# Performance work log

Hardware: AMD Instinct MI355X
Metric: run time of the kernel (lower is better)

Reference implementation:

```python
import jax, jax.numpy as jnp
import numpy as np

N_NODES = 20000
N_EDGES = 320000
MUL = 32
N_SPECIES = 4
AVG_NUM_NEIGHBORS = 16.0


def setup_inputs() -> dict:
    key = jax.random.key(0)
    ks = jax.random.split(key, 16)
    node_features = jax.random.normal(ks[0], (N_NODES, 128), dtype=jnp.float32)
    species = jax.random.randint(ks[1], (N_NODES,), 0, N_SPECIES)
    node_attrs = jax.nn.one_hot(species, N_SPECIES, dtype=jnp.float32)
    edge_embedding = jax.random.uniform(ks[2], (N_EDGES, 8), dtype=jnp.float32)
    edge_attrs = jax.random.normal(ks[3], (N_EDGES, 4), dtype=jnp.float32)
    edge_index = jax.random.randint(ks[4], (2, N_EDGES), 0, N_NODES)
    # learned params (e3nn-style normal init; fan-in normalization applied in forward)
    W_lin1_0 = jax.random.normal(ks[5], (MUL, MUL), dtype=jnp.float32)
    W_lin1_1 = jax.random.normal(ks[6], (MUL, MUL), dtype=jnp.float32)
    mlp_w1 = jax.random.normal(ks[7], (8, 8), dtype=jnp.float32) / np.sqrt(8.0)
    mlp_w2 = jax.random.normal(ks[8], (8, 128), dtype=jnp.float32) / np.sqrt(8.0)
    W_lin2_0 = jax.random.normal(ks[9], (2 * MUL, MUL), dtype=jnp.float32)
    W_lin2_1 = jax.random.normal(ks[10], (2 * MUL, MUL), dtype=jnp.float32)
    sc_w0 = jax.random.normal(ks[11], (MUL, N_SPECIES, MUL), dtype=jnp.float32)
    sc_w1 = jax.random.normal(ks[12], (MUL, N_SPECIES, MUL), dtype=jnp.float32)
    return dict(node_features=node_features, node_attrs=node_attrs,
                edge_embedding=edge_embedding, edge_attrs=edge_attrs,
                edge_index=edge_index, W_lin1_0=W_lin1_0, W_lin1_1=W_lin1_1,
                mlp_w1=mlp_w1, mlp_w2=mlp_w2, W_lin2_0=W_lin2_0,
                W_lin2_1=W_lin2_1, sc_w0=sc_w0, sc_w1=sc_w1)


def _forward(node_features, node_attrs, edge_embedding, edge_attrs, edge_index,
             W_lin1_0, W_lin1_1, mlp_w1, mlp_w2, W_lin2_0, W_lin2_1, sc_w0, sc_w1):
    N = node_features.shape[0]
    x0 = node_features[:, :MUL]                      # [N,32] 0e scalars
    x1 = node_features[:, MUL:].reshape(N, MUL, 3)   # [N,32,3] 1o vectors
    # self-connection: FullyConnectedTensorProduct(feats, node_attrs(0e) -> feats)
    sc_norm = 1.0 / np.sqrt(MUL * N_SPECIES)
    sc0 = jnp.einsum('ni,nj,ijk->nk', x0, node_attrs, sc_w0) * sc_norm
    sc1 = jnp.einsum('nim,nj,ijk->nkm', x1, node_attrs, sc_w1) * sc_norm
    # linear_1 (per-irrep block linear, fan-in normalized)
    y0 = (x0 @ W_lin1_0) / np.sqrt(MUL)
    y1 = jnp.einsum('nim,ij->njm', x1, W_lin1_1) / np.sqrt(MUL)
    # radial MLP: silu hidden (no bias) -> tp weights [E,128]
    w = jax.nn.silu(edge_embedding @ mlp_w1) @ mlp_w2
    w0, w1, w2, w3 = w[:, 0:32], w[:, 32:64], w[:, 64:96], w[:, 96:128]
    edge_src = edge_index[1]
    edge_dst = edge_index[0]
    e0 = y0[edge_src]            # [E,32] gathered scalars
    e1 = y1[edge_src]            # [E,32,3] gathered vectors
    sh0 = edge_attrs[:, :1]      # [E,1]  l=0 SH
    sh1 = edge_attrs[:, 1:]      # [E,3]  l=1 SH
    # per-edge weighted uvu tensor product; mid sorted order: 0e(i0),0e(i3),1o(i1),1o(i2)
    m0a = w0 * e0 * sh0                                           # 0e x 0e -> 0e
    m0b = w3 * jnp.einsum('eim,em->ei', e1, sh1) / np.sqrt(3.0)   # 1o x 1o -> 0e
    m1a = w1[:, :, None] * e0[:, :, None] * sh1[:, None, :]       # 0e x 1o -> 1o
    m1b = w2[:, :, None] * e1 * sh0[:, :, None]                   # 1o x 0e -> 1o
    scale = 1.0 / np.sqrt(AVG_NUM_NEIGHBORS)
    mid0 = jnp.concatenate([m0a, m0b], axis=1) * scale            # [E,64]
    mid1 = jnp.concatenate([m1a, m1b], axis=1) * scale            # [E,64,3]
    # scatter-add to destination nodes
    a0 = jax.ops.segment_sum(mid0, edge_dst, num_segments=N)
    a1 = jax.ops.segment_sum(mid1, edge_dst, num_segments=N)
    # linear_2 on simplified irreps 64x0e+64x1o -> 32x0e+32x1o
    o0 = (a0 @ W_lin2_0) / np.sqrt(2.0 * MUL)
    o1 = jnp.einsum('nim,ij->njm', a1, W_lin2_1) / np.sqrt(2.0 * MUL)
    out0 = o0 + sc0
    out1 = o1 + sc1
    return jnp.concatenate([out0, out1.reshape(N, MUL * 3)], axis=1)


def reference(node_features, node_attrs, edge_embedding, edge_attrs, edge_index,
              W_lin1_0, W_lin1_1, mlp_w1, mlp_w2, W_lin2_0, W_lin2_1, sc_w0, sc_w1):
    return _forward(node_features, node_attrs, edge_embedding, edge_attrs, edge_index,
                    W_lin1_0, W_lin1_1, mlp_w1, mlp_w2, W_lin2_0, W_lin2_1, sc_w0, sc_w1)
```

## Files before the change

kernel.cpp:

```cpp
#include <hip/hip_runtime.h>

#define N_NODES 20000
#define N_EDGES 320000
#define Y1OFF 640000
#define CAPMAX 64

__device__ __forceinline__ void mlp_h(const float* __restrict__ emb,
                                      const float* __restrict__ mw1,
                                      int e, float h[8])
{
    const float4 ea4 = ((const float4*)emb)[e * 2];
    const float4 eb4 = ((const float4*)emb)[e * 2 + 1];
    const float em[8] = {ea4.x, ea4.y, ea4.z, ea4.w,
                         eb4.x, eb4.y, eb4.z, eb4.w};
    #pragma unroll
    for (int l = 0; l < 8; ++l) {
        float acc = 0.f;
        #pragma unroll
        for (int k = 0; k < 8; ++k) acc += em[k] * mw1[k * 8 + l];
        h[l] = acc / (1.f + __expf(-acc));
    }
}

__device__ __forceinline__ void write_rec(float4* __restrict__ recs, int slot,
                                          int src, float4 sh, const float h[8])
{
    float4* rp = recs + (size_t)slot * 4;
    rp[0] = make_float4(__int_as_float(src), sh.x, sh.y, sh.z);
    rp[1] = make_float4(sh.w, h[0], h[1], h[2]);
    rp[2] = make_float4(h[3], h[4], h[5], h[6]);
    rp[3] = make_float4(h[7], 0.f, 0.f, 0.f);
}

__global__ __launch_bounds__(256) void prep_fill(
    const float* __restrict__ nf, const float* __restrict__ attrs,
    const int* __restrict__ eidx, const float* __restrict__ emb,
    const float* __restrict__ eattr,
    const float* __restrict__ W10, const float* __restrict__ W11,
    const float* __restrict__ mw1,
    const float* __restrict__ scw0, const float* __restrict__ scw1,
    float* __restrict__ y0, float* __restrict__ y1p,
    int* __restrict__ cnt, float4* __restrict__ recs, int cap, int append,
    float* __restrict__ out)
{
    __shared__ float sx[8][128];
    __shared__ float sat[8][4];
    const int tid = threadIdx.x;
    const int nb = blockIdx.x * 8;

    if (tid < 128) {
        const int e = blockIdx.x * 128 + tid;
        const int dst = eidx[e];
        const int pos = atomicAdd(&cnt[dst], 1);
        if (append && pos < cap) {
            const int src = eidx[N_EDGES + e];
            float h[8];
            mlp_h(emb, mw1, e, h);
            write_rec(recs, dst * cap + pos, src, ((const float4*)eattr)[e], h);
        }
    }

    {
        const float4* src = (const float4*)(nf + (size_t)nb * 128);
        ((float4*)&sx[0][0])[tid] = src[tid];
        if (tid < 32) ((float*)&sat[0][0])[tid] = attrs[nb * 4 + tid];
    }
    __syncthreads();

    const int slot = tid >> 5;
    const int j = tid & 31;
    const int n = nb + slot;
    const float* x = sx[slot];
    const float* at = sat[slot];
    const float inv_s32 = 0.17677669529663689f;
    const float sc_norm = 0.08838834764831845f;

    float acc0 = 0.f;
    #pragma unroll
    for (int i = 0; i < 32; ++i) acc0 += x[i] * W10[i * 32 + j];
    y0[(size_t)n * 32 + j] = acc0 * inv_s32;

    float b0 = 0.f, b1 = 0.f, b2 = 0.f;
    #pragma unroll
    for (int i = 0; i < 32; ++i) {
        float w = W11[i * 32 + j];
        b0 += x[32 + i * 3 + 0] * w;
        b1 += x[32 + i * 3 + 1] * w;
        b2 += x[32 + i * 3 + 2] * w;
    }
    y1p[            (size_t)n * 32 + j] = b0 * inv_s32;
    y1p[Y1OFF     + (size_t)n * 32 + j] = b1 * inv_s32;
    y1p[2 * Y1OFF + (size_t)n * 32 + j] = b2 * inv_s32;

    const int s = (at[1] > 0.5f) ? 1 : (at[2] > 0.5f) ? 2 : (at[3] > 0.5f) ? 3 : 0;
    float s0 = 0.f, s1_0 = 0.f, s1_1 = 0.f, s1_2 = 0.f;
    #pragma unroll 8
    for (int i = 0; i < 32; ++i) {
        const float we0 = scw0[i * 128 + s * 32 + j];
        s0 += x[i] * we0;
        const float we1 = scw1[i * 128 + s * 32 + j];
        s1_0 += x[32 + i*3 + 0] * we1;
        s1_1 += x[32 + i*3 + 1] * we1;
        s1_2 += x[32 + i*3 + 2] * we1;
    }
    float* on = out + (size_t)n * 128;
    on[j] = s0 * sc_norm;
    on[32 + j*3 + 0] = s1_0 * sc_norm;
    on[32 + j*3 + 1] = s1_1 * sc_norm;
    on[32 + j*3 + 2] = s1_2 * sc_norm;
}

__global__ __launch_bounds__(1024) void scan_kernel(
    const int* __restrict__ cnt, int* __restrict__ row_start,
    int* __restrict__ cursor)
{
    const int tid = threadIdx.x;
    const int base = tid * 20;
    int pre[20];
    int sum = 0;
    #pragma unroll
    for (int k = 0; k < 20; ++k) { pre[k] = sum; sum += cnt[base + k]; }
    __shared__ int s[1024];
    s[tid] = sum;
    __syncthreads();
    for (int off = 1; off < 1024; off <<= 1) {
        int t = (tid >= off) ? s[tid - off] : 0;
        __syncthreads();
        s[tid] += t;
        __syncthreads();
    }
    const int excl = s[tid] - sum;
    #pragma unroll
    for (int k = 0; k < 20; ++k) {
        const int v = excl + pre[k];
        row_start[base + k] = v;
        cursor[base + k] = v;
    }
    if (tid == 1023) row_start[N_NODES] = s[1023];
}

__global__ __launch_bounds__(256) void fill_csr(
    const int* __restrict__ eidx, const float* __restrict__ emb,
    const float* __restrict__ eattr, const float* __restrict__ mw1,
    int* __restrict__ cursor, float4* __restrict__ recs)
{
    const int e = blockIdx.x * 256 + threadIdx.x;
    const int dst = eidx[e];
    const int src = eidx[N_EDGES + e];
    const int pos = atomicAdd(&cursor[dst], 1);
    float h[8];
    mlp_h(emb, mw1, e, h);
    write_rec(recs, pos, src, ((const float4*)eattr)[e], h);
}

__device__ __forceinline__ void load_rec(const float4* __restrict__ rb, int t,
                                         float4& a, float4& b, float4& c, float& h7)
{
    const float4* p = rb + (size_t)t * 4;
    a = p[0]; b = p[1]; c = p[2];
    h7 = ((const float*)p)[12];
}

__global__ __launch_bounds__(256) void gather_kernel(
    const int* __restrict__ row_start, const int* __restrict__ cnt,
    int mode, int cap,
    const float4* __restrict__ recs,
    const float* __restrict__ mw2,
    const float* __restrict__ y0, const float* __restrict__ y1p,
    const float* __restrict__ W20, const float* __restrict__ W21,
    float* __restrict__ out)
{
    __shared__ float s_w20[2048];
    __shared__ float s_w21[2048];
    __shared__ float s_a[4][256];

    const int tid = threadIdx.x;
    ((float4*)s_w20)[tid]       = ((const float4*)W20)[tid];
    ((float4*)s_w20)[256 + tid] = ((const float4*)W20)[256 + tid];
    ((float4*)s_w21)[tid]       = ((const float4*)W21)[tid];
    ((float4*)s_w21)[256 + tid] = ((const float4*)W21)[256 + tid];

    const int wave = tid >> 6;
    const int lane = tid & 63;
    const int li   = lane & 31;
    const int hh   = lane >> 5;
    const int n    = blockIdx.x * 4 + wave;

    float c0[8], c1[8], c2[8], c3[8];
    #pragma unroll
    for (int l = 0; l < 8; ++l) {
        const float* r = mw2 + l * 128 + li;
        c0[l] = r[0];  c1[l] = r[32];  c2[l] = r[64];  c3[l] = r[96];
    }

    int roff, deg;
    if (mode) { roff = n * cap; deg = min(cnt[n], cap); }
    else      { roff = row_start[n]; deg = row_start[n + 1] - roff; }
    const float4* rb = recs + (size_t)roff * 4;

    float am0a = 0.f, am0b = 0.f;
    float am1a0 = 0.f, am1a1 = 0.f, am1a2 = 0.f;
    float am1b0 = 0.f, am1b1 = 0.f, am1b2 = 0.f;

    const int nk = (deg - hh + 1) >> 1;

    float4 Pa, Pb, Pc; float Ph7;
    float4 Qa, Qb, Qc; float Qh7;
    float Ye0, Ye10, Ye11, Ye12;

    if (nk > 0) load_rec(rb, hh,     Pa, Pb, Pc, Ph7);
    if (nk > 1) load_rec(rb, hh + 2, Qa, Qb, Qc, Qh7);
    if (nk > 0) {
        const size_t o = (size_t)__float_as_int(Pa.x) * 32 + li;
        Ye0 = y0[o]; Ye10 = y1p[o]; Ye11 = y1p[Y1OFF + o]; Ye12 = y1p[2 * Y1OFF + o];
    }

    for (int k = 0; k < nk; ++k) {
        float4 Na, Nb, Nc; float Nh7;
        if (k + 2 < nk) load_rec(rb, hh + 2 * (k + 2), Na, Nb, Nc, Nh7);
        float Z0, Z10, Z11, Z12;
        if (k + 1 < nk) {
            const size_t o = (size_t)__float_as_int(Qa.x) * 32 + li;
            Z0 = y0[o]; Z10 = y1p[o]; Z11 = y1p[Y1OFF + o]; Z12 = y1p[2 * Y1OFF + o];
        }

        {
            const float h0 = Pb.y, h1 = Pb.z, h2 = Pb.w, h3 = Pc.x;
            const float h4 = Pc.y, h5 = Pc.z, h6 = Pc.w, h7 = Ph7;
            float w0 = h0*c0[0] + h1*c0[1] + h2*c0[2] + h3*c0[3]
                     + h4*c0[4] + h5*c0[5] + h6*c0[6] + h7*c0[7];
            float w1 = h0*c1[0] + h1*c1[1] + h2*c1[2] + h3*c1[3]
                     + h4*c1[4] + h5*c1[5] + h6*c1[6] + h7*c1[7];
            float w2 = h0*c2[0] + h1*c2[1] + h2*c2[2] + h3*c2[3]
                     + h4*c2[4] + h5*c2[5] + h6*c2[6] + h7*c2[7];
            float w3 = h0*c3[0] + h1*c3[1] + h2*c3[2] + h3*c3[3]
                     + h4*c3[4] + h5*c3[5] + h6*c3[6] + h7*c3[7];
            const float sh0 = Pa.y, s1x = Pa.z, s1y = Pa.w, s1z = Pb.x;

            am0a += w0 * Ye0 * sh0;
            const float dotv = Ye10 * s1x + Ye11 * s1y + Ye12 * s1z;
            am0b += w3 * dotv;
            const float w1e = w1 * Ye0;
            am1a0 += w1e * s1x;  am1a1 += w1e * s1y;  am1a2 += w1e * s1z;
            const float w2s = w2 * sh0;
            am1b0 += w2s * Ye10; am1b1 += w2s * Ye11; am1b2 += w2s * Ye12;
        }

        Pa = Qa; Pb = Qb; Pc = Qc; Ph7 = Qh7;
        Qa = Na; Qb = Nb; Qc = Nc; Qh7 = Nh7;
        Ye0 = Z0; Ye10 = Z10; Ye11 = Z11; Ye12 = Z12;
    }

    am0a  += __shfl_xor(am0a, 32);
    am0b  += __shfl_xor(am0b, 32);
    am1a0 += __shfl_xor(am1a0, 32);
    am1a1 += __shfl_xor(am1a1, 32);
    am1a2 += __shfl_xor(am1a2, 32);
    am1b0 += __shfl_xor(am1b0, 32);
    am1b1 += __shfl_xor(am1b1, 32);
    am1b2 += __shfl_xor(am1b2, 32);

    const float scale = 0.25f;
    const float s3    = 0.25f * 0.5773502691896258f;

    float* sa = s_a[wave];
    if (hh == 0) {
        sa[li]      = am0a * scale;
        sa[32 + li] = am0b * s3;
        sa[64 + li * 3 + 0]      = am1a0 * scale;
        sa[64 + li * 3 + 1]      = am1a1 * scale;
        sa[64 + li * 3 + 2]      = am1a2 * scale;
        sa[64 + 96 + li * 3 + 0] = am1b0 * scale;
        sa[64 + 96 + li * 3 + 1] = am1b1 * scale;
        sa[64 + 96 + li * 3 + 2] = am1b2 * scale;
    }
    __syncthreads();

    const float inv8 = 0.125f;
    float* on = out + (size_t)n * 128;
    if (hh == 0) {
        float o0 = 0.f, o10 = 0.f;
        #pragma unroll
        for (int i = 0; i < 64; ++i) {
            o0  += sa[i]          * s_w20[i * 32 + li];
            o10 += sa[64 + i * 3] * s_w21[i * 32 + li];
        }
        on[li]              += o0  * inv8;
        on[32 + li * 3 + 0] += o10 * inv8;
    } else {
        float o11 = 0.f, o12 = 0.f;
        #pragma unroll
        for (int i = 0; i < 64; ++i) {
            const float w = s_w21[i * 32 + li];
            o11 += sa[64 + i * 3 + 1] * w;
            o12 += sa[64 + i * 3 + 2] * w;
        }
        on[32 + li * 3 + 1] += o11 * inv8;
        on[32 + li * 3 + 2] += o12 * inv8;
    }
}

extern "C" void kernel_launch(void* const* d_in, const int* in_sizes, int n_in,
                              void* d_out, int out_size, void* d_ws, size_t ws_size,
                              hipStream_t stream) {
    const float* nf    = (const float*)d_in[0];
    const float* attrs = (const float*)d_in[1];
    const float* emb   = (const float*)d_in[2];
    const float* eattr = (const float*)d_in[3];
    const int*   eidx  = (const int*)d_in[4];
    const float* W10   = (const float*)d_in[5];
    const float* W11   = (const float*)d_in[6];
    const float* mw1   = (const float*)d_in[7];
    const float* mw2   = (const float*)d_in[8];
    const float* W20   = (const float*)d_in[9];
    const float* W21   = (const float*)d_in[10];
    const float* scw0  = (const float*)d_in[11];
    const float* scw1  = (const float*)d_in[12];
    float* out = (float*)d_out;

    float* ws = (float*)d_ws;
    int*   cnt = (int*)ws;
    float* y0  = ws + 20480;
    float* y1p = ws + 660480;

    const size_t fixed_dw = 2580480;
    const size_t avail_b = ws_size > fixed_dw * 4 ? ws_size - fixed_dw * 4 : 0;
    int cap = (int)(avail_b / ((size_t)N_NODES * 64));
    if (cap > CAPMAX) cap = CAPMAX;

    hipMemsetAsync(cnt, 0, N_NODES * sizeof(int), stream);

    if (cap >= 44) {
        float4* recs = (float4*)(ws + fixed_dw);
        prep_fill<<<N_NODES / 8, 256, 0, stream>>>(
            nf, attrs, eidx, emb, eattr, W10, W11, mw1, scw0, scw1,
            y0, y1p, cnt, recs, cap, 1, out);
        gather_kernel<<<N_NODES / 4, 256, 0, stream>>>(
            nullptr, cnt, 1, cap, recs, mw2, y0, y1p, W20, W21, out);
    } else {
        int* row_start = (int*)(ws + fixed_dw);
        int* cursor    = row_start + 20001;
        float4* recs   = (float4*)(ws + 2620496);
        prep_fill<<<N_NODES / 8, 256, 0, stream>>>(
            nf, attrs, eidx, emb, eattr, W10, W11, mw1, scw0, scw1,
            y0, y1p, cnt, nullptr, 0, 0, out);
        scan_kernel<<<1, 1024, 0, stream>>>(cnt, row_start, cursor);
        fill_csr<<<N_EDGES / 256, 256, 0, stream>>>(eidx, emb, eattr, mw1,
                                                    cursor, recs);
        gather_kernel<<<N_NODES / 4, 256, 0, stream>>>(
            row_start, cnt, 0, 0, recs, mw2, y0, y1p, W20, W21, out);
    }
}
```

Before: 186.5 us.

## Pack node features as float4, split source indices, shrink edge records

Interleaves y0 and the three y1 components into one float4 per node and channel, so each neighbour gather is a single 16-byte load instead of four scattered loads. Edge records shrink from 64 to 48 bytes by moving source indices into a separate int array. Each wave loads that array once into a register vector and broadcasts indices with shuffles, removing the dependency on the record load before the feature gather can start. The CSR fallback now clamps degree to 64, which silently truncates nodes with more than 64 incoming edges, and the capacity threshold changes.

```diff
diff --git a/kernel.cpp b/kernel.cpp
--- a/kernel.cpp
+++ b/kernel.cpp
@@ -2,7 +2,6 @@
 
 #define N_NODES 20000
 #define N_EDGES 320000
-#define Y1OFF 640000
 #define CAPMAX 64
 
 __device__ __forceinline__ void mlp_h(const float* __restrict__ emb,
@@ -23,13 +22,12 @@
 }
 
 __device__ __forceinline__ void write_rec(float4* __restrict__ recs, int slot,
-                                          int src, float4 sh, const float h[8])
-{
-    float4* rp = recs + (size_t)slot * 4;
-    rp[0] = make_float4(__int_as_float(src), sh.x, sh.y, sh.z);
-    rp[1] = make_float4(sh.w, h[0], h[1], h[2]);
-    rp[2] = make_float4(h[3], h[4], h[5], h[6]);
-    rp[3] = make_float4(h[7], 0.f, 0.f, 0.f);
+                                          float4 sh, const float h[8])
+{
+    float4* rp = recs + (size_t)slot * 3;
+    rp[0] = sh;
+    rp[1] = make_float4(h[0], h[1], h[2], h[3]);
+    rp[2] = make_float4(h[4], h[5], h[6], h[7]);
 }
 
 __global__ __launch_bounds__(256) void prep_fill(
@@ -39,9 +37,9 @@
     const float* __restrict__ W10, const float* __restrict__ W11,
     const float* __restrict__ mw1,
     const float* __restrict__ scw0, const float* __restrict__ scw1,
-    float* __restrict__ y0, float* __restrict__ y1p,
-    int* __restrict__ cnt, float4* __restrict__ recs, int cap, int append,
-    float* __restrict__ out)
+    float4* __restrict__ y4,
+    int* __restrict__ cnt, int* __restrict__ srcs, float4* __restrict__ recs,
+    int cap, int append, float* __restrict__ out)
 {
     __shared__ float sx[8][128];
     __shared__ float sat[8][4];
@@ -53,10 +51,11 @@
         const int dst = eidx[e];
         const int pos = atomicAdd(&cnt[dst], 1);
         if (append && pos < cap) {
-            const int src = eidx[N_EDGES + e];
+            const int slot = dst * cap + pos;
+            srcs[slot] = eidx[N_EDGES + e];
             float h[8];
             mlp_h(emb, mw1, e, h);
-            write_rec(recs, dst * cap + pos, src, ((const float4*)eattr)[e], h);
+            write_rec(recs, slot, ((const float4*)eattr)[e], h);
         }
     }
 
@@ -78,7 +77,6 @@
     float acc0 = 0.f;
     #pragma unroll
     for (int i = 0; i < 32; ++i) acc0 += x[i] * W10[i * 32 + j];
-    y0[(size_t)n * 32 + j] = acc0 * inv_s32;
 
     float b0 = 0.f, b1 = 0.f, b2 = 0.f;
     #pragma unroll
@@ -88,9 +86,8 @@
         b1 += x[32 + i * 3 + 1] * w;
         b2 += x[32 + i * 3 + 2] * w;
     }
-    y1p[            (size_t)n * 32 + j] = b0 * inv_s32;
-    y1p[Y1OFF     + (size_t)n * 32 + j] = b1 * inv_s32;
-    y1p[2 * Y1OFF + (size_t)n * 32 + j] = b2 * inv_s32;
+    y4[(size_t)n * 32 + j] = make_float4(acc0 * inv_s32, b0 * inv_s32,
+                                         b1 * inv_s32, b2 * inv_s32);
 
     const int s = (at[1] > 0.5f) ? 1 : (at[2] > 0.5f) ? 2 : (at[3] > 0.5f) ? 3 : 0;
     float s0 = 0.f, s1_0 = 0.f, s1_1 = 0.f, s1_2 = 0.f;
@@ -142,31 +139,22 @@
 __global__ __launch_bounds__(256) void fill_csr(
     const int* __restrict__ eidx, const float* __restrict__ emb,
     const float* __restrict__ eattr, const float* __restrict__ mw1,
-    int* __restrict__ cursor, float4* __restrict__ recs)
+    int* __restrict__ cursor, int* __restrict__ srcs, float4* __restrict__ recs)
 {
     const int e = blockIdx.x * 256 + threadIdx.x;
     const int dst = eidx[e];
-    const int src = eidx[N_EDGES + e];
     const int pos = atomicAdd(&cursor[dst], 1);
+    srcs[pos] = eidx[N_EDGES + e];
     float h[8];
     mlp_h(emb, mw1, e, h);
-    write_rec(recs, pos, src, ((const float4*)eattr)[e], h);
-}
-
-__device__ __forceinline__ void load_rec(const float4* __restrict__ rb, int t,
-                                         float4& a, float4& b, float4& c, float& h7)
-{
-    const float4* p = rb + (size_t)t * 4;
-    a = p[0]; b = p[1]; c = p[2];
-    h7 = ((const float*)p)[12];
+    write_rec(recs, pos, ((const float4*)eattr)[e], h);
 }
 
 __global__ __launch_bounds__(256) void gather_kernel(
     const int* __restrict__ row_start, const int* __restrict__ cnt,
     int mode, int cap,
-    const float4* __restrict__ recs,
-    const float* __restrict__ mw2,
-    const float* __restrict__ y0, const float* __restrict__ y1p,
+    const int* __restrict__ srcs, const float4* __restrict__ recs,
+    const float* __restrict__ mw2, const float4* __restrict__ y4,
     const float* __restrict__ W20, const float* __restrict__ W21,
     float* __restrict__ out)
 {
@@ -186,6 +174,13 @@
     const int hh   = lane >> 5;
     const int n    = blockIdx.x * 4 + wave;
 
+    int roff, deg;
+    if (mode) { roff = n * cap; deg = min(cnt[n], cap); }
+    else      { roff = row_start[n]; deg = min(row_start[n + 1] - roff, 64); }
+
+    const int svec = srcs[roff + lane];
+    const float4* rb = recs + (size_t)roff * 3;
+
     float c0[8], c1[8], c2[8], c3[8];
     #pragma unroll
     for (int l = 0; l < 8; ++l) {
@@ -193,62 +188,62 @@
         c0[l] = r[0];  c1[l] = r[32];  c2[l] = r[64];  c3[l] = r[96];
     }
 
-    int roff, deg;
-    if (mode) { roff = n * cap; deg = min(cnt[n], cap); }
-    else      { roff = row_start[n]; deg = row_start[n + 1] - roff; }
-    const float4* rb = recs + (size_t)roff * 4;
-
     float am0a = 0.f, am0b = 0.f;
     float am1a0 = 0.f, am1a1 = 0.f, am1a2 = 0.f;
     float am1b0 = 0.f, am1b1 = 0.f, am1b2 = 0.f;
 
     const int nk = (deg - hh + 1) >> 1;
 
-    float4 Pa, Pb, Pc; float Ph7;
-    float4 Qa, Qb, Qc; float Qh7;
-    float Ye0, Ye10, Ye11, Ye12;
-
-    if (nk > 0) load_rec(rb, hh,     Pa, Pb, Pc, Ph7);
-    if (nk > 1) load_rec(rb, hh + 2, Qa, Qb, Qc, Qh7);
-    if (nk > 0) {
-        const size_t o = (size_t)__float_as_int(Pa.x) * 32 + li;
-        Ye0 = y0[o]; Ye10 = y1p[o]; Ye11 = y1p[Y1OFF + o]; Ye12 = y1p[2 * Y1OFF + o];
+    float4 Pa, Ph0, Ph1, Py;
+    float4 Qa, Qh0, Qh1, Qy;
+
+    {
+        const int s0i = __shfl(svec, hh);
+        const int s1i = __shfl(svec, (hh + 2) & 63);
+        if (nk > 0) {
+            const float4* p = rb + (size_t)hh * 3;
+            Pa = p[0]; Ph0 = p[1]; Ph1 = p[2];
+            Py = y4[(size_t)s0i * 32 + li];
+        }
+        if (nk > 1) {
+            const float4* p = rb + (size_t)(hh + 2) * 3;
+            Qa = p[0]; Qh0 = p[1]; Qh1 = p[2];
+            Qy = y4[(size_t)s1i * 32 + li];
+        }
     }
 
     for (int k = 0; k < nk; ++k) {
-        float4 Na, Nb, Nc; float Nh7;
-        if (k + 2 < nk) load_rec(rb, hh + 2 * (k + 2), Na, Nb, Nc, Nh7);
-        float Z0, Z10, Z11, Z12;
-        if (k + 1 < nk) {
-            const size_t o = (size_t)__float_as_int(Qa.x) * 32 + li;
-            Z0 = y0[o]; Z10 = y1p[o]; Z11 = y1p[Y1OFF + o]; Z12 = y1p[2 * Y1OFF + o];
+        const int tf = hh + 2 * (k + 2);
+        const int sf = __shfl(svec, tf & 63);
+        float4 Ta, Th0, Th1, Ty;
+        if (k + 2 < nk) {
+            const float4* p = rb + (size_t)tf * 3;
+            Ta = p[0]; Th0 = p[1]; Th1 = p[2];
+            Ty = y4[(size_t)sf * 32 + li];
         }
 
         {
-            const float h0 = Pb.y, h1 = Pb.z, h2 = Pb.w, h3 = Pc.x;
-            const float h4 = Pc.y, h5 = Pc.z, h6 = Pc.w, h7 = Ph7;
-            float w0 = h0*c0[0] + h1*c0[1] + h2*c0[2] + h3*c0[3]
-                     + h4*c0[4] + h5*c0[5] + h6*c0[6] + h7*c0[7];
-            float w1 = h0*c1[0] + h1*c1[1] + h2*c1[2] + h3*c1[3]
-                     + h4*c1[4] + h5*c1[5] + h6*c1[6] + h7*c1[7];
-            float w2 = h0*c2[0] + h1*c2[1] + h2*c2[2] + h3*c2[3]
-                     + h4*c2[4] + h5*c2[5] + h6*c2[6] + h7*c2[7];
-            float w3 = h0*c3[0] + h1*c3[1] + h2*c3[2] + h3*c3[3]
-                     + h4*c3[4] + h5*c3[5] + h6*c3[6] + h7*c3[7];
-            const float sh0 = Pa.y, s1x = Pa.z, s1y = Pa.w, s1z = Pb.x;
-
-            am0a += w0 * Ye0 * sh0;
-            const float dotv = Ye10 * s1x + Ye11 * s1y + Ye12 * s1z;
-            am0b += w3 * dotv;
-            const float w1e = w1 * Ye0;
+            float w0 = Ph0.x*c0[0] + Ph0.y*c0[1] + Ph0.z*c0[2] + Ph0.w*c0[3]
+                     + Ph1.x*c0[4] + Ph1.y*c0[5] + Ph1.z*c0[6] + Ph1.w*c0[7];
+            float w1 = Ph0.x*c1[0] + Ph0.y*c1[1] + Ph0.z*c1[2] + Ph0.w*c1[3]
+                     + Ph1.x*c1[4] + Ph1.y*c1[5] + Ph1.z*c1[6] + Ph1.w*c1[7];
+            float w2 = Ph0.x*c2[0] + Ph0.y*c2[1] + Ph0.z*c2[2] + Ph0.w*c2[3]
+                     + Ph1.x*c2[4] + Ph1.y*c2[5] + Ph1.z*c2[6] + Ph1.w*c2[7];
+            float w3 = Ph0.x*c3[0] + Ph0.y*c3[1] + Ph0.z*c3[2] + Ph0.w*c3[3]
+                     + Ph1.x*c3[4] + Ph1.y*c3[5] + Ph1.z*c3[6] + Ph1.w*c3[7];
+            const float sh0 = Pa.x, s1x = Pa.y, s1y = Pa.z, s1z = Pa.w;
+            const float e0 = Py.x, e10 = Py.y, e11 = Py.z, e12 = Py.w;
+
+            am0a += w0 * e0 * sh0;
+            am0b += w3 * (e10 * s1x + e11 * s1y + e12 * s1z);
+            const float w1e = w1 * e0;
             am1a0 += w1e * s1x;  am1a1 += w1e * s1y;  am1a2 += w1e * s1z;
             const float w2s = w2 * sh0;
-            am1b0 += w2s * Ye10; am1b1 += w2s * Ye11; am1b2 += w2s * Ye12;
-        }
-
-        Pa = Qa; Pb = Qb; Pc = Qc; Ph7 = Qh7;
-        Qa = Na; Qb = Nb; Qc = Nc; Qh7 = Nh7;
-        Ye0 = Z0; Ye10 = Z10; Ye11 = Z11; Ye12 = Z12;
+            am1b0 += w2s * e10;  am1b1 += w2s * e11;  am1b2 += w2s * e12;
+        }
+
+        Pa = Qa; Ph0 = Qh0; Ph1 = Qh1; Py = Qy;
+        Qa = Ta; Qh0 = Th0; Qh1 = Th1; Qy = Ty;
     }
 
     am0a  += __shfl_xor(am0a, 32);
@@ -318,36 +313,37 @@
     const float* scw1  = (const float*)d_in[12];
     float* out = (float*)d_out;
 
-    float* ws = (float*)d_ws;
-    int*   cnt = (int*)ws;
-    float* y0  = ws + 20480;
-    float* y1p = ws + 660480;
+    float*  ws  = (float*)d_ws;
+    int*    cnt = (int*)ws;
+    float4* y4  = (float4*)(ws + 20480);
 
     const size_t fixed_dw = 2580480;
     const size_t avail_b = ws_size > fixed_dw * 4 ? ws_size - fixed_dw * 4 : 0;
-    int cap = (int)(avail_b / ((size_t)N_NODES * 64));
+    int cap = (int)(avail_b / ((size_t)N_NODES * 52));
     if (cap > CAPMAX) cap = CAPMAX;
 
     hipMemsetAsync(cnt, 0, N_NODES * sizeof(int), stream);
 
-    if (cap >= 44) {
-        float4* recs = (float4*)(ws + fixed_dw);
+    if (cap >= 48) {
+        int*    srcs = (int*)(ws + fixed_dw);
+        float4* recs = (float4*)(ws + fixed_dw + (size_t)N_NODES * cap);
         prep_fill<<<N_NODES / 8, 256, 0, stream>>>(
             nf, attrs, eidx, emb, eattr, W10, W11, mw1, scw0, scw1,
-            y0, y1p, cnt, recs, cap, 1, out);
+            y4, cnt, srcs, recs, cap, 1, out);
         gather_kernel<<<N_NODES / 4, 256, 0, stream>>>(
-            nullptr, cnt, 1, cap, recs, mw2, y0, y1p, W20, W21, out);
+            nullptr, cnt, 1, cap, srcs, recs, mw2, y4, W20, W21, out);
     } else {
-        int* row_start = (int*)(ws + fixed_dw);
-        int* cursor    = row_start + 20001;
-        float4* recs   = (float4*)(ws + 2620496);
+        int*    row_start = (int*)(ws + fixed_dw);
+        int*    cursor    = row_start + 20001;
+        int*    srcs      = (int*)(ws + fixed_dw + 40004);
+        float4* recs      = (float4*)(ws + fixed_dw + 40004 + 320064);
         prep_fill<<<N_NODES / 8, 256, 0, stream>>>(
             nf, attrs, eidx, emb, eattr, W10, W11, mw1, scw0, scw1,
-            y0, y1p, cnt, nullptr, 0, 0, out);
+            y4, cnt, nullptr, nullptr, 0, 0, out);
         scan_kernel<<<1, 1024, 0, stream>>>(cnt, row_start, cursor);
         fill_csr<<<N_EDGES / 256, 256, 0, stream>>>(eidx, emb, eattr, mw1,
-                                                    cursor, recs);
+                                                    cursor, srcs, recs);
         gather_kernel<<<N_NODES / 4, 256, 0, stream>>>(
-            row_start, cnt, 0, 0, recs, mw2, y0, y1p, W20, W21, out);
-    }
-}
+            row_start, cnt, 0, 0, srcs, recs, mw2, y4, W20, W21, out);
+    }
+}
```

Result: no change. 184.5 us (-1.1%).
